# Kernel optimization log

Measured on AMD Instinct MI355X. Metric: run time of the kernel, lower is better.

The kernel has to match this reference:

```python
import jax, jax.numpy as jnp
import numpy as np

N = 30000
DEG = 16
E_RAND = N * DEG
E = E_RAND + N  # with self loops appended
T = 2
F_IN, H1, OUT = 128, 128, 64
NBSZ = 15
AGG = 0.8
NEG_SLOPE = 0.2


def setup_inputs() -> dict:
    key = jax.random.key(0)
    ks = jax.random.split(key, 10)
    x_all = jax.random.normal(ks[0], (T, N, F_IN), dtype=jnp.float32)
    # edges per snapshot: random edges + self loops (mirrors remove_self_loops + add_self_loops)
    loops = jnp.arange(N, dtype=jnp.int32)
    eis = []
    for t in range(T):
        src = jax.random.randint(jax.random.fold_in(ks[1], t), (E_RAND,), 0, N, dtype=jnp.int32)
        dst = jax.random.randint(jax.random.fold_in(ks[2], t), (E_RAND,), 0, N, dtype=jnp.int32)
        eis.append(jnp.stack([jnp.concatenate([src, loops]), jnp.concatenate([dst, loops])]))
    edge_index_all = jnp.stack(eis)  # [T, 2, E]
    def glorot(k, shape):
        fan = shape[0] + shape[-1]
        s = jnp.sqrt(6.0 / fan)
        return jax.random.uniform(k, shape, jnp.float32, -s, s)
    W1 = glorot(ks[3], (F_IN, 2 * H1))
    att1 = glorot(ks[4], (1, 1, 4 * H1))   # [1, heads=1, 2*out_neurons]
    b1 = jnp.zeros((2 * H1,), jnp.float32)
    W2 = glorot(ks[5], (H1, 2 * OUT))
    att2 = glorot(ks[6], (1, 1, 4 * OUT))
    b2 = jnp.zeros((2 * OUT,), jnp.float32)
    return {"x_all": x_all, "edge_index_all": edge_index_all,
            "W1": W1, "att1": att1, "b1": b1, "W2": W2, "att2": att2, "b2": b2}


def _conv(x, edge_index, W, att, b, C):
    """One DGIBConv (heads=1, Bernoulli distribution, diag reparam, eval mode).
    Returns (node_out [N,C], ixz scalar, structure_kl scalar)."""
    h = x @ W                                    # [N, 2C]
    src, dst = edge_index[0], edge_index[1]
    x_j = h[src]                                 # [E, 2C] per-edge gather (source)
    x_i = h[dst]                                 # [E, 2C] target
    a = att[0, 0]                                # [4C]
    logits = jnp.sum(x_i * a[:2 * C], -1) + jnp.sum(x_j * a[2 * C:], -1)  # [E]
    logits = jax.nn.leaky_relu(logits, NEG_SLOPE)
    # Bernoulli branch: softmax of ones over segments == 1/deg(dst)
    deg = jax.ops.segment_sum(jnp.ones_like(logits), dst, num_segments=N)  # [N]
    norm = 1.0 / deg[dst]
    p = jnp.clip(jax.nn.sigmoid(logits), 0.01, 0.99)  # posterior Bernoulli probs
    alpha = p * norm
    aggr = jax.ops.segment_sum(x_j * alpha[:, None], dst, num_segments=N) + b  # [N, 2C]
    # diag reparam: mean || std-logit split; Gaussian prior N(0, I)
    mu = aggr[:, :C]
    std = jax.nn.softplus(aggr[:, C:]) + 1e-10
    kl = -jnp.log(std) + 0.5 * (std * std + mu * mu) - 0.5  # KL(N(mu,std)||N(0,1)) per dim
    ixz = jnp.mean(jnp.sum(kl, -1))
    # structure KL: Bernoulli(p) || Bernoulli(logits = 1/nbsz)
    q = jax.nn.sigmoid(jnp.float32(1.0 / NBSZ))
    skl = jnp.mean(p * jnp.log(p / q) + (1.0 - p) * jnp.log((1.0 - p) / (1.0 - q)))
    return mu, ixz, skl


def _layer(x_list, edge_index_all, W, att, b, C):
    """Temporal DGIBConv.forward: per-snapshot conv + weighted temporal fusion."""
    outs, ixzs, skls = [], [], []
    for t in range(T):
        out, ixz, skl = _conv(x_list[t], edge_index_all[t], W, att, b, C)
        if t > 0:
            w = jax.nn.sigmoid(jnp.arange(t, dtype=jnp.float32))[:, None, None]  # [t,1,1]
            prev = jnp.stack(outs[:t])                                           # [t,N,C]
            out = jnp.sum(w * prev, 0) / t * AGG + out * (1.0 - AGG)
        outs.append(out)
        ixzs.append(ixz)
        skls.append(skl)
    return outs, jnp.mean(jnp.stack(ixzs)), jnp.mean(jnp.stack(skls))


def reference(x_all, edge_index_all, W1, att1, b1, W2, att2, b2):
    xs = [x_all[t] for t in range(T)]
    h1, ixz1, skl1 = _layer(xs, edge_index_all, W1, att1, b1, H1)
    h1 = [jax.nn.relu(h) for h in h1]  # with_relu=True, eval -> dropout is identity
    h2, ixz2, skl2 = _layer(h1, edge_index_all, W2, att2, b2, OUT)
    out = jnp.stack(h2)                # [T, N, OUT]
    ixz_mean = (ixz1 + ixz2) / 2.0
    skl_mean = (skl1 + skl2) / 2.0
    return out, ixz_mean, skl_mean
```

## Files before the change

### kernel.cpp

```cpp
#include <hip/hip_runtime.h>
#include <hip/hip_bf16.h>
#include <hip/hip_fp8.h>

#define N_NODES 30000
#define N_EDGES 510000
#define K_DIM   128
#define ABLK    7500

typedef short bf16x8 __attribute__((ext_vector_type(8)));
typedef float f32x4  __attribute__((ext_vector_type(4)));
typedef float f32x2  __attribute__((ext_vector_type(2)));
typedef unsigned int u32x2 __attribute__((ext_vector_type(2)));

__device__ __forceinline__ unsigned short f2bf(float f) {
  __hip_bfloat16 h = __float2bfloat16(f);
  return *(unsigned short*)&h;
}
__device__ __forceinline__ unsigned char f2fp8(float f) {
  __hip_fp8_e4m3 q(f);
  return (unsigned char)q.__x;
}

__global__ void transpose_w_kernel(const float* __restrict__ W1, unsigned short* __restrict__ Wt1,
                                   const float* __restrict__ W2, unsigned short* __restrict__ Wt2) {
  int i = blockIdx.x * blockDim.x + threadIdx.x;
  if (i < 128 * 256) {
    int k = i >> 8, m = i & 255;
    Wt1[m * 128 + k] = f2bf(W1[i]);
  } else if (i < 128 * 256 + 128 * 128) {
    int j = i - 128 * 256;
    int k = j >> 7, m = j & 127;
    Wt2[m * 128 + k] = f2bf(W2[j]);
  }
}

__global__ void deg_kernel(const int* __restrict__ ei, int* __restrict__ deg0,
                           int* __restrict__ deg1, int e) {
  int i = blockIdx.x * blockDim.x + threadIdx.x;
  if (i < 2 * e) {
    int t = i >= e ? 1 : 0;
    int j = i - t * e;
    int d = ei[(size_t)t * 2 * e + e + j];
    atomicAdd(&(t ? deg1 : deg0)[d], 1);
  }
}

__global__ __launch_bounds__(1024) void scan_kernel(const int* __restrict__ deg0, int* __restrict__ off0, int* __restrict__ cur0,
                                                    const int* __restrict__ deg1, int* __restrict__ off1, int* __restrict__ cur1,
                                                    int n) {
  const int* deg = blockIdx.x ? deg1 : deg0;
  int* off = blockIdx.x ? off1 : off0;
  int* cur = blockIdx.x ? cur1 : cur0;
  const int CHUNK = 30;
  __shared__ int wsum[16];
  int tid = threadIdx.x;
  int base = tid * CHUNK;
  int sum = 0;
  for (int i = 0; i < CHUNK; i++)
    if (base + i < n) sum += deg[base + i];
  int lane = tid & 63, wid = tid >> 6;
  int incl = sum;
#pragma unroll
  for (int o = 1; o < 64; o <<= 1) {
    int v = __shfl_up(incl, o);
    if (lane >= o) incl += v;
  }
  if (lane == 63) wsum[wid] = incl;
  __syncthreads();
  if (tid == 0) {
    int run = 0;
    for (int w = 0; w < 16; w++) { int v = wsum[w]; wsum[w] = run; run += v; }
  }
  __syncthreads();
  int run = incl - sum + wsum[wid];
  for (int i = 0; i < CHUNK; i++) {
    if (base + i < n) {
      off[base + i] = run;
      cur[base + i] = run;
      run += deg[base + i];
    }
  }
}

__global__ void scatter_kernel(const int* __restrict__ ei,
                               int* __restrict__ cur0, int* __restrict__ cur1,
                               int* __restrict__ csr0, int* __restrict__ csr1, int e) {
  int i = blockIdx.x * blockDim.x + threadIdx.x;
  if (i < 2 * e) {
    int t = i >= e ? 1 : 0;
    int j = i - t * e;
    int s = ei[(size_t)t * 2 * e + j];
    int d = ei[(size_t)t * 2 * e + e + j];
    int* cur = t ? cur1 : cur0;
    int* csr = t ? csr1 : csr0;
    int p = atomicAdd(&cur[d], 1);
    csr[p] = s;
  }
}

template<int M, bool F32IN>
__global__ __launch_bounds__(256) void gemm_kernel(const void* __restrict__ X0v,
                                                   const void* __restrict__ X1v,
                                                   const short* __restrict__ Wt,
                                                   unsigned char* __restrict__ H0,
                                                   unsigned char* __restrict__ H1,
                                                   const float* __restrict__ att,
                                                   float* __restrict__ si0, float* __restrict__ si1,
                                                   float* __restrict__ sj0, float* __restrict__ sj1,
                                                   int nrows) {
  int t = blockIdx.y;
  const void* Xv = t ? X1v : X0v;
  unsigned char* Hf8 = t ? H1 : H0;
  float* s_i = t ? si1 : si0;
  float* s_j = t ? sj1 : sj0;

  int wave = blockIdx.x * 4 + (threadIdx.x >> 6);
  int lane = threadIdx.x & 63;
  if (wave * 16 >= nrows) return;
  int m16 = lane & 15, quad = lane >> 4;

  bf16x8 a[4];
  size_t arow = (size_t)(wave * 16 + m16) * K_DIM + quad * 8;
  if constexpr (F32IN) {
    const float* X = (const float*)Xv;
#pragma unroll
    for (int kc = 0; kc < 4; kc++) {
      f32x4 lo = *(const f32x4*)(X + arow + kc * 32);
      f32x4 hi = *(const f32x4*)(X + arow + kc * 32 + 4);
#pragma unroll
      for (int j = 0; j < 4; j++) {
        ((unsigned short*)&a[kc])[j]     = f2bf(lo[j]);
        ((unsigned short*)&a[kc])[4 + j] = f2bf(hi[j]);
      }
    }
  } else {
    const short* X = (const short*)Xv;
#pragma unroll
    for (int kc = 0; kc < 4; kc++) a[kc] = *(const bf16x8*)(X + arow + kc * 32);
  }

  float sip[4] = {0.f, 0.f, 0.f, 0.f}, sjp[4] = {0.f, 0.f, 0.f, 0.f};
#pragma unroll
  for (int nt = 0; nt < M / 16; nt++) {
    f32x4 acc = {0.f, 0.f, 0.f, 0.f};
    size_t brow = (size_t)(nt * 16 + m16) * K_DIM + quad * 8;
#pragma unroll
    for (int kc = 0; kc < 4; kc++) {
      bf16x8 b = *(const bf16x8*)(Wt + brow + kc * 32);
      acc = __builtin_amdgcn_mfma_f32_16x16x32_bf16(a[kc], b, acc, 0, 0, 0);
    }
    int col = nt * 16 + m16;
    float aA = att[col], aB = att[M + col];
#pragma unroll
    for (int r = 0; r < 4; r++) {
      int row = wave * 16 + quad * 4 + r;
      Hf8[(size_t)row * M + col] = f2fp8(acc[r]);
      sip[r] += acc[r] * aA;
      sjp[r] += acc[r] * aB;
    }
  }
#pragma unroll
  for (int o = 1; o < 16; o <<= 1) {
#pragma unroll
    for (int r = 0; r < 4; r++) {
      sip[r] += __shfl_xor(sip[r], o);
      sjp[r] += __shfl_xor(sjp[r], o);
    }
  }
  if (m16 == 0) {
#pragma unroll
    for (int r = 0; r < 4; r++) {
      int row = wave * 16 + quad * 4 + r;
      s_i[row] = sip[r];
      s_j[row] = sjp[r];
    }
  }
}

template<int M>
__global__ __launch_bounds__(256) void aggr_kernel(const unsigned char* __restrict__ H0,
                                                   const unsigned char* __restrict__ H1,
                                                   const int* __restrict__ csr0, const int* __restrict__ csr1,
                                                   const int* __restrict__ off0, const int* __restrict__ off1,
                                                   const int* __restrict__ deg0, const int* __restrict__ deg1,
                                                   const float* __restrict__ si0, const float* __restrict__ si1,
                                                   const float* __restrict__ sj0, const float* __restrict__ sj1,
                                                   const float* __restrict__ bias,
                                                   float* __restrict__ mu0, float* __restrict__ mu1,
                                                   f32x2* __restrict__ partials,
                                                   int n) {
  constexpr int C = M / 2;
  constexpr int LPR = M / 8;
  constexpr int LOG2LPR = (M == 256) ? 5 : 4;
  constexpr int EPL = 64 / LPR;
  constexpr int NL = 4;
  constexpr int U = NL * EPL;

  int t = blockIdx.y;
  const unsigned char* Hf8 = t ? H1 : H0;
  const int* csr = t ? csr1 : csr0;
  const int* off = t ? off1 : off0;
  const int* deg = t ? deg1 : deg0;
  const float* s_i = t ? si1 : si0;
  const float* s_j = t ? sj1 : sj0;
  float* mu = t ? mu1 : mu0;

  __shared__ float red_i[4], red_s[4];
  int wid = threadIdx.x >> 6, lane = threadIdx.x & 63;
  int wave = blockIdx.x * 4 + wid;
  float ixz = 0.f, skl = 0.f;

  if (wave < n) {
    int d     = __builtin_amdgcn_readfirstlane(deg[wave]);
    int start = __builtin_amdgcn_readfirstlane(off[wave]);
    float si  = s_i[wave];
    float norm = 1.0f / (float)d;
    int sub = lane & (LPR - 1);
    int g   = lane >> LOG2LPR;
    int c0  = sub * 8;
    const float q   = 1.0f / (1.0f + __expf(-(1.0f / 15.0f)));
    const float lq  = __logf(q);
    const float l1q = __logf(1.0f - q);

    float acc[8];
#pragma unroll
    for (int k = 0; k < 8; k++) acc[k] = 0.f;

    for (int e0 = 0; e0 < d; e0 += U) {
      int ee = e0 + lane;
      bool val = (lane < U) && (ee < d);
      int ap = start + (val ? ee : (d - 1));
      int idxl = csr[ap];
      float sjl = s_j[idxl];
      float lg = si + sjl;
      lg = lg > 0.f ? lg : 0.2f * lg;
      float p = 1.0f / (1.0f + __expf(-lg));
      p = fminf(fmaxf(p, 0.01f), 0.99f);
      float wl = val ? p : 0.f;
      if (val)
        skl += p * (__logf(p) - lq) + (1.0f - p) * (__logf(1.0f - p) - l1q);

      u32x2 hv[NL];
      float wsel[NL];
#pragma unroll
      for (int l = 0; l < NL; l++) {
        int idx; float wv_;
        if constexpr (EPL == 2) {
          int i0 = __shfl(idxl, l * 2), i1 = __shfl(idxl, l * 2 + 1);
          float w0 = __shfl(wl, l * 2), w1 = __shfl(wl, l * 2 + 1);
          idx = g ? i1 : i0;
          wv_ = g ? w1 : w0;
        } else {
          int i0 = __shfl(idxl, l * 4),     i1 = __shfl(idxl, l * 4 + 1);
          int i2 = __shfl(idxl, l * 4 + 2), i3 = __shfl(idxl, l * 4 + 3);
          float w0 = __shfl(wl, l * 4),     w1 = __shfl(wl, l * 4 + 1);
          float w2 = __shfl(wl, l * 4 + 2), w3 = __shfl(wl, l * 4 + 3);
          int ia = (g & 1) ? i1 : i0, ib = (g & 1) ? i3 : i2;
          idx = (g & 2) ? ib : ia;
          float fa = (g & 1) ? w1 : w0, fb = (g & 1) ? w3 : w2;
          wv_ = (g & 2) ? fb : fa;
        }
        wsel[l] = wv_;
        hv[l] = *(const u32x2*)(Hf8 + (size_t)idx * M + c0);
      }
#pragma unroll
      for (int l = 0; l < NL; l++) {
        f32x2 d0 = __builtin_amdgcn_cvt_pk_f32_fp8((int)hv[l][0], false);
        f32x2 d1 = __builtin_amdgcn_cvt_pk_f32_fp8((int)hv[l][0], true);
        f32x2 d2 = __builtin_amdgcn_cvt_pk_f32_fp8((int)hv[l][1], false);
        f32x2 d3 = __builtin_amdgcn_cvt_pk_f32_fp8((int)hv[l][1], true);
        float wv_ = wsel[l];
        acc[0] += wv_ * d0[0]; acc[1] += wv_ * d0[1];
        acc[2] += wv_ * d1[0]; acc[3] += wv_ * d1[1];
        acc[4] += wv_ * d2[0]; acc[5] += wv_ * d2[1];
        acc[6] += wv_ * d3[0]; acc[7] += wv_ * d3[1];
      }
    }

#pragma unroll
    for (int o = LPR; o < 64; o <<= 1) {
#pragma unroll
      for (int k = 0; k < 8; k++) acc[k] += __shfl_xor(acc[k], o);
    }

    if (lane < LPR) {
      if (c0 < C) {
        f32x4 m0, m1;
#pragma unroll
        for (int k = 0; k < 4; k++) {
          float a = acc[k] * norm + bias[c0 + k];
          m0[k] = a;
          ixz += 0.5f * a * a - 0.5f;
        }
#pragma unroll
        for (int k = 0; k < 4; k++) {
          float a = acc[4 + k] * norm + bias[c0 + 4 + k];
          m1[k] = a;
          ixz += 0.5f * a * a - 0.5f;
        }
        *(f32x4*)(mu + (size_t)wave * C + c0) = m0;
        *(f32x4*)(mu + (size_t)wave * C + c0 + 4) = m1;
      } else {
#pragma unroll
        for (int k = 0; k < 8; k++) {
          float a = acc[k] * norm + bias[c0 + k];
          float sp = (a > 20.f) ? a : log1pf(__expf(a));
          sp += 1e-10f;
          ixz += -__logf(sp) + 0.5f * sp * sp;
        }
      }
    }
  }
#pragma unroll
  for (int o = 32; o > 0; o >>= 1) {
    ixz += __shfl_xor(ixz, o);
    skl += __shfl_xor(skl, o);
  }
  if (lane == 0) { red_i[wid] = ixz; red_s[wid] = skl; }
  __syncthreads();
  if (threadIdx.x == 0) {
    f32x2 pr;
    pr[0] = red_i[0] + red_i[1] + red_i[2] + red_i[3];
    pr[1] = red_s[0] + red_s[1] + red_s[2] + red_s[3];
    partials[t * ABLK + blockIdx.x] = pr;
  }
}

__global__ void fuse1_kernel(const float* __restrict__ mu0, const float* __restrict__ mu1,
                             __hip_bfloat16* __restrict__ x0, __hip_bfloat16* __restrict__ x1, int n) {
  int i = blockIdx.x * blockDim.x + threadIdx.x;
  if (i < n) {
    float m0 = mu0[i], m1 = mu1[i];
    x0[i] = __float2bfloat16(fmaxf(m0, 0.f));
    x1[i] = __float2bfloat16(fmaxf(0.4f * m0 + 0.2f * m1, 0.f));
  }
}

__global__ void fuse2_kernel(const float* __restrict__ mu0, const float* __restrict__ mu1,
                             float* __restrict__ out, int n) {
  int i = blockIdx.x * blockDim.x + threadIdx.x;
  if (i < n) {
    float m0 = mu0[i], m1 = mu1[i];
    out[i] = m0;
    out[n + i] = 0.4f * m0 + 0.2f * m1;
  }
}

__global__ __launch_bounds__(1024) void reduce_kernel(const f32x2* __restrict__ p1,
                                                      const f32x2* __restrict__ p2,
                                                      float* __restrict__ out2) {
  __shared__ float ri[16], rs[16];
  float ixz = 0.f, skl = 0.f;
  for (int i = threadIdx.x; i < 2 * ABLK; i += 1024) {
    f32x2 a = p1[i], b = p2[i];
    ixz += a[0] + b[0];
    skl += a[1] + b[1];
  }
  int lane = threadIdx.x & 63, wid = threadIdx.x >> 6;
#pragma unroll
  for (int o = 32; o > 0; o >>= 1) {
    ixz += __shfl_xor(ixz, o);
    skl += __shfl_xor(skl, o);
  }
  if (lane == 0) { ri[wid] = ixz; rs[wid] = skl; }
  __syncthreads();
  if (threadIdx.x == 0) {
    float si = 0.f, ss = 0.f;
    for (int w = 0; w < 16; w++) { si += ri[w]; ss += rs[w]; }
    out2[0] = si / (4.0f * (float)N_NODES);
    out2[1] = ss / (4.0f * (float)N_EDGES);
  }
}

extern "C" void kernel_launch(void* const* d_in, const int* in_sizes, int n_in,
                              void* d_out, int out_size, void* d_ws, size_t ws_size,
                              hipStream_t stream) {
  const float* x_all = (const float*)d_in[0];
  const int* ei      = (const int*)d_in[1];
  const float* W1    = (const float*)d_in[2];
  const float* att1  = (const float*)d_in[3];
  const float* b1    = (const float*)d_in[4];
  const float* W2    = (const float*)d_in[5];
  const float* att2  = (const float*)d_in[6];
  const float* b2    = (const float*)d_in[7];
  float* out         = (float*)d_out;

  char* ws = (char*)d_ws;
  size_t off = 0;
  auto alloc = [&](size_t bytes) {
    char* p = ws + off;
    off = (off + bytes + 255) & ~(size_t)255;
    return p;
  };
  unsigned short* wt1  = (unsigned short*)alloc(256 * 128 * sizeof(short));
  unsigned short* wt2  = (unsigned short*)alloc(128 * 128 * sizeof(short));
  unsigned char* hf8_0 = (unsigned char*)alloc((size_t)N_NODES * 256);
  unsigned char* hf8_1 = (unsigned char*)alloc((size_t)N_NODES * 256);
  float* si0   = (float*)alloc(N_NODES * sizeof(float));
  float* si1   = (float*)alloc(N_NODES * sizeof(float));
  float* sj0   = (float*)alloc(N_NODES * sizeof(float));
  float* sj1   = (float*)alloc(N_NODES * sizeof(float));
  float* mu1_0 = (float*)alloc((size_t)N_NODES * 128 * sizeof(float));
  float* mu1_1 = (float*)alloc((size_t)N_NODES * 128 * sizeof(float));
  __hip_bfloat16* x2_0 = (__hip_bfloat16*)alloc((size_t)N_NODES * 128 * sizeof(short));
  __hip_bfloat16* x2_1 = (__hip_bfloat16*)alloc((size_t)N_NODES * 128 * sizeof(short));
  float* mu2_0 = mu1_0;
  float* mu2_1 = mu1_0 + (size_t)N_NODES * 64;
  int* degp[2]  = {(int*)alloc(N_NODES * 4), (int*)alloc(N_NODES * 4)};
  int* offp[2]  = {(int*)alloc(N_NODES * 4), (int*)alloc(N_NODES * 4)};
  int* curp[2]  = {(int*)alloc(N_NODES * 4), (int*)alloc(N_NODES * 4)};
  int* csrp[2]  = {(int*)alloc(N_EDGES * 4), (int*)alloc(N_EDGES * 4)};
  f32x2* part1  = (f32x2*)alloc(2 * ABLK * sizeof(f32x2));
  f32x2* part2  = (f32x2*)alloc(2 * ABLK * sizeof(f32x2));

  hipMemsetAsync(degp[0], 0, N_NODES * 4, stream);
  hipMemsetAsync(degp[1], 0, N_NODES * 4, stream);

  transpose_w_kernel<<<192, 256, 0, stream>>>(W1, wt1, W2, wt2);

  deg_kernel<<<(2 * N_EDGES + 255) / 256, 256, 0, stream>>>(ei, degp[0], degp[1], N_EDGES);
  scan_kernel<<<2, 1024, 0, stream>>>(degp[0], offp[0], curp[0], degp[1], offp[1], curp[1], N_NODES);
  scatter_kernel<<<(2 * N_EDGES + 255) / 256, 256, 0, stream>>>(ei, curp[0], curp[1],
                                                                csrp[0], csrp[1], N_EDGES);

  dim3 ggrid(469, 2), agrid(ABLK, 2);

  const float* x0 = x_all;
  const float* x1 = x_all + (size_t)N_NODES * K_DIM;
  gemm_kernel<256, true><<<ggrid, 256, 0, stream>>>(x0, x1, (const short*)wt1, hf8_0, hf8_1,
                                                    att1, si0, si1, sj0, sj1, N_NODES);
  aggr_kernel<256><<<agrid, 256, 0, stream>>>(hf8_0, hf8_1, csrp[0], csrp[1], offp[0], offp[1],
                                              degp[0], degp[1], si0, si1, sj0, sj1, b1,
                                              mu1_0, mu1_1, part1, N_NODES);
  fuse1_kernel<<<(N_NODES * 128 + 255) / 256, 256, 0, stream>>>(mu1_0, mu1_1, x2_0, x2_1, N_NODES * 128);

  gemm_kernel<128, false><<<ggrid, 256, 0, stream>>>(x2_0, x2_1, (const short*)wt2, hf8_0, hf8_1,
                                                     att2, si0, si1, sj0, sj1, N_NODES);
  aggr_kernel<128><<<agrid, 256, 0, stream>>>(hf8_0, hf8_1, csrp[0], csrp[1], offp[0], offp[1],
                                              degp[0], degp[1], si0, si1, sj0, sj1, b2,
                                              mu2_0, mu2_1, part2, N_NODES);
  fuse2_kernel<<<(N_NODES * 64 + 255) / 256, 256, 0, stream>>>(mu2_0, mu2_1, out, N_NODES * 64);
  reduce_kernel<<<1, 1024, 0, stream>>>(part1, part2, out + (size_t)2 * N_NODES * 64);
}
```

Baseline: 602.6 us.

## Split edge weight computation into separate edge kernel and pipeline aggregation loads

After: 811.6 us. 34.7% more time.

```diff
diff --git a/kernel.cpp b/kernel.cpp
--- a/kernel.cpp
+++ b/kernel.cpp
@@ -1,11 +1,11 @@
 #include <hip/hip_runtime.h>
 #include <hip/hip_bf16.h>
-#include <hip/hip_fp8.h>
 
 #define N_NODES 30000
 #define N_EDGES 510000
 #define K_DIM   128
 #define ABLK    7500
+#define EBLK    997
 
 typedef short bf16x8 __attribute__((ext_vector_type(8)));
 typedef float f32x4  __attribute__((ext_vector_type(4)));
@@ -15,10 +15,6 @@
 __device__ __forceinline__ unsigned short f2bf(float f) {
   __hip_bfloat16 h = __float2bfloat16(f);
   return *(unsigned short*)&h;
-}
-__device__ __forceinline__ unsigned char f2fp8(float f) {
-  __hip_fp8_e4m3 q(f);
-  return (unsigned char)q.__x;
 }
 
 __global__ void transpose_w_kernel(const float* __restrict__ W1, unsigned short* __restrict__ Wt1,
@@ -45,12 +41,15 @@
   }
 }
 
-__global__ __launch_bounds__(1024) void scan_kernel(const int* __restrict__ deg0, int* __restrict__ off0, int* __restrict__ cur0,
-                                                    const int* __restrict__ deg1, int* __restrict__ off1, int* __restrict__ cur1,
+__global__ __launch_bounds__(1024) void scan_kernel(const int* __restrict__ deg0, int* __restrict__ off0,
+                                                    int* __restrict__ cur0, float* __restrict__ rn0,
+                                                    const int* __restrict__ deg1, int* __restrict__ off1,
+                                                    int* __restrict__ cur1, float* __restrict__ rn1,
                                                     int n) {
   const int* deg = blockIdx.x ? deg1 : deg0;
   int* off = blockIdx.x ? off1 : off0;
   int* cur = blockIdx.x ? cur1 : cur0;
+  float* rn = blockIdx.x ? rn1 : rn0;
   const int CHUNK = 30;
   __shared__ int wsum[16];
   int tid = threadIdx.x;
@@ -75,16 +74,18 @@
   int run = incl - sum + wsum[wid];
   for (int i = 0; i < CHUNK; i++) {
     if (base + i < n) {
+      int dg = deg[base + i];
       off[base + i] = run;
       cur[base + i] = run;
-      run += deg[base + i];
+      rn[base + i] = 1.0f / (float)dg;
+      run += dg;
     }
   }
 }
 
 __global__ void scatter_kernel(const int* __restrict__ ei,
                                int* __restrict__ cur0, int* __restrict__ cur1,
-                               int* __restrict__ csr0, int* __restrict__ csr1, int e) {
+                               unsigned int* __restrict__ csr0, unsigned int* __restrict__ csr1, int e) {
   int i = blockIdx.x * blockDim.x + threadIdx.x;
   if (i < 2 * e) {
     int t = i >= e ? 1 : 0;
@@ -92,9 +93,9 @@
     int s = ei[(size_t)t * 2 * e + j];
     int d = ei[(size_t)t * 2 * e + e + j];
     int* cur = t ? cur1 : cur0;
-    int* csr = t ? csr1 : csr0;
+    unsigned int* csr = t ? csr1 : csr0;
     int p = atomicAdd(&cur[d], 1);
-    csr[p] = s;
+    csr[p] = (unsigned int)s | ((unsigned int)d << 16);
   }
 }
 
@@ -154,7 +155,8 @@
 #pragma unroll
     for (int r = 0; r < 4; r++) {
       int row = wave * 16 + quad * 4 + r;
-      Hf8[(size_t)row * M + col] = f2fp8(acc[r]);
+      int pk = __builtin_amdgcn_cvt_pk_fp8_f32(acc[r], acc[r], 0, false);
+      Hf8[(size_t)row * M + col] = (unsigned char)pk;
       sip[r] += acc[r] * aA;
       sjp[r] += acc[r] * aB;
     }
@@ -177,153 +179,196 @@
   }
 }
 
+__global__ __launch_bounds__(256) void edge_kernel(const unsigned int* __restrict__ csr_0,
+                                                   const unsigned int* __restrict__ csr_1,
+                                                   const float* __restrict__ rn0, const float* __restrict__ rn1,
+                                                   const float* __restrict__ si0, const float* __restrict__ si1,
+                                                   const float* __restrict__ sj0, const float* __restrict__ sj1,
+                                                   u32x2* __restrict__ iw0, u32x2* __restrict__ iw1,
+                                                   float* __restrict__ epart,
+                                                   int e) {
+  int t = blockIdx.y;
+  const unsigned int* csr = t ? csr_1 : csr_0;
+  const float* rn = t ? rn1 : rn0;
+  const float* s_i = t ? si1 : si0;
+  const float* s_j = t ? sj1 : sj0;
+  u32x2* iw = t ? iw1 : iw0;
+
+  const float q   = 1.0f / (1.0f + __expf(-(1.0f / 15.0f)));
+  const float lq  = __logf(q);
+  const float l1q = __logf(1.0f - q);
+
+  __shared__ float red[4];
+  float skl = 0.f;
+  int p0 = (blockIdx.x * 256 + threadIdx.x) * 2;
+#pragma unroll
+  for (int u = 0; u < 2; u++) {
+    int p = p0 + u;
+    if (p < e) {
+      unsigned int sd = csr[p];
+      int s = (int)(sd & 0xffffu);
+      int dd = (int)(sd >> 16);
+      float lg = s_i[dd] + s_j[s];
+      lg = lg > 0.f ? lg : 0.2f * lg;
+      float pv = 1.0f / (1.0f + __expf(-lg));
+      pv = fminf(fmaxf(pv, 0.01f), 0.99f);
+      skl += pv * (__logf(pv) - lq) + (1.0f - pv) * (__logf(1.0f - pv) - l1q);
+      float w = pv * rn[dd];
+      u32x2 o;
+      o[0] = (unsigned int)s;
+      o[1] = __float_as_uint(w);
+      iw[p] = o;
+    }
+  }
+  int lane = threadIdx.x & 63, wid = threadIdx.x >> 6;
+#pragma unroll
+  for (int o = 32; o > 0; o >>= 1) skl += __shfl_xor(skl, o);
+  if (lane == 0) red[wid] = skl;
+  __syncthreads();
+  if (threadIdx.x == 0) epart[t * EBLK + blockIdx.x] = red[0] + red[1] + red[2] + red[3];
+}
+
 template<int M>
 __global__ __launch_bounds__(256) void aggr_kernel(const unsigned char* __restrict__ H0,
                                                    const unsigned char* __restrict__ H1,
-                                                   const int* __restrict__ csr0, const int* __restrict__ csr1,
+                                                   const u32x2* __restrict__ iw0, const u32x2* __restrict__ iw1,
                                                    const int* __restrict__ off0, const int* __restrict__ off1,
                                                    const int* __restrict__ deg0, const int* __restrict__ deg1,
-                                                   const float* __restrict__ si0, const float* __restrict__ si1,
-                                                   const float* __restrict__ sj0, const float* __restrict__ sj1,
                                                    const float* __restrict__ bias,
                                                    float* __restrict__ mu0, float* __restrict__ mu1,
-                                                   f32x2* __restrict__ partials,
+                                                   float* __restrict__ apart,
                                                    int n) {
   constexpr int C = M / 2;
-  constexpr int LPR = M / 8;
-  constexpr int LOG2LPR = (M == 256) ? 5 : 4;
+  constexpr int LPR = M / 16;
+  constexpr int L2LPR = (M == 256) ? 4 : 3;
   constexpr int EPL = 64 / LPR;
-  constexpr int NL = 4;
-  constexpr int U = NL * EPL;
-
-  int t = blockIdx.y;
+  constexpr int U = 16;
+  constexpr int NL = U / EPL;
+
+  int bid = blockIdx.x;
+  int xcd = bid & 7;
+  int t = xcd >> 2;
+  int nb = (bid >> 3) * 4 + (xcd & 3);
+
   const unsigned char* Hf8 = t ? H1 : H0;
-  const int* csr = t ? csr1 : csr0;
+  const u32x2* iw = t ? iw1 : iw0;
   const int* off = t ? off1 : off0;
   const int* deg = t ? deg1 : deg0;
-  const float* s_i = t ? si1 : si0;
-  const float* s_j = t ? sj1 : sj0;
   float* mu = t ? mu1 : mu0;
 
-  __shared__ float red_i[4], red_s[4];
+  __shared__ float red_i[4];
   int wid = threadIdx.x >> 6, lane = threadIdx.x & 63;
-  int wave = blockIdx.x * 4 + wid;
-  float ixz = 0.f, skl = 0.f;
+  int wave = nb * 4 + wid;
+  float ixz = 0.f;
 
   if (wave < n) {
     int d     = __builtin_amdgcn_readfirstlane(deg[wave]);
     int start = __builtin_amdgcn_readfirstlane(off[wave]);
-    float si  = s_i[wave];
-    float norm = 1.0f / (float)d;
+    const u32x2* iwp = iw + start;
     int sub = lane & (LPR - 1);
-    int g   = lane >> LOG2LPR;
-    int c0  = sub * 8;
-    const float q   = 1.0f / (1.0f + __expf(-(1.0f / 15.0f)));
-    const float lq  = __logf(q);
-    const float l1q = __logf(1.0f - q);
-
-    float acc[8];
-#pragma unroll
-    for (int k = 0; k < 8; k++) acc[k] = 0.f;
-
-    for (int e0 = 0; e0 < d; e0 += U) {
-      int ee = e0 + lane;
-      bool val = (lane < U) && (ee < d);
-      int ap = start + (val ? ee : (d - 1));
-      int idxl = csr[ap];
-      float sjl = s_j[idxl];
-      float lg = si + sjl;
-      lg = lg > 0.f ? lg : 0.2f * lg;
-      float p = 1.0f / (1.0f + __expf(-lg));
-      p = fminf(fmaxf(p, 0.01f), 0.99f);
-      float wl = val ? p : 0.f;
-      if (val)
-        skl += p * (__logf(p) - lq) + (1.0f - p) * (__logf(1.0f - p) - l1q);
-
-      u32x2 hv[NL];
-      float wsel[NL];
+    int g   = lane >> L2LPR;
+    int c0  = sub * 16;
+    const unsigned char* hbase = Hf8 + c0;
+
+    f32x2 acc[8];
+#pragma unroll
+    for (int k = 0; k < 8; k++) acc[k] = {0.f, 0.f};
+
+    u32x2 iwr[NL];
+    uint4 hv0[NL], hv1[NL];
+    float w0[NL], w1[NL];
+
+    auto LOADIW = [&](int base) {
 #pragma unroll
       for (int l = 0; l < NL; l++) {
-        int idx; float wv_;
-        if constexpr (EPL == 2) {
-          int i0 = __shfl(idxl, l * 2), i1 = __shfl(idxl, l * 2 + 1);
-          float w0 = __shfl(wl, l * 2), w1 = __shfl(wl, l * 2 + 1);
-          idx = g ? i1 : i0;
-          wv_ = g ? w1 : w0;
-        } else {
-          int i0 = __shfl(idxl, l * 4),     i1 = __shfl(idxl, l * 4 + 1);
-          int i2 = __shfl(idxl, l * 4 + 2), i3 = __shfl(idxl, l * 4 + 3);
-          float w0 = __shfl(wl, l * 4),     w1 = __shfl(wl, l * 4 + 1);
-          float w2 = __shfl(wl, l * 4 + 2), w3 = __shfl(wl, l * 4 + 3);
-          int ia = (g & 1) ? i1 : i0, ib = (g & 1) ? i3 : i2;
-          idx = (g & 2) ? ib : ia;
-          float fa = (g & 1) ? w1 : w0, fb = (g & 1) ? w3 : w2;
-          wv_ = (g & 2) ? fb : fa;
+        int e = base + l * EPL + g;
+        e = e < d ? e : d - 1;
+        iwr[l] = iwp[e];
+      }
+    };
+    auto ISSUE = [&](uint4* hv) {
+#pragma unroll
+      for (int l = 0; l < NL; l++)
+        hv[l] = *(const uint4*)(hbase + (size_t)iwr[l][0] * M);
+    };
+    auto EXTW = [&](float* w, int base) {
+#pragma unroll
+      for (int l = 0; l < NL; l++) {
+        int e = base + l * EPL + g;
+        w[l] = (e < d) ? __uint_as_float(iwr[l][1]) : 0.f;
+      }
+    };
+    auto FMA = [&](uint4* hv, float* w) {
+#pragma unroll
+      for (int l = 0; l < NL; l++) {
+        f32x2 wv = {w[l], w[l]};
+#pragma unroll
+        for (int k = 0; k < 4; k++) {
+          f32x2 lo = __builtin_amdgcn_cvt_pk_f32_fp8((int)hv[l][k], false);
+          f32x2 hi = __builtin_amdgcn_cvt_pk_f32_fp8((int)hv[l][k], true);
+          acc[2 * k]     = lo * wv + acc[2 * k];
+          acc[2 * k + 1] = hi * wv + acc[2 * k + 1];
         }
-        wsel[l] = wv_;
-        hv[l] = *(const u32x2*)(Hf8 + (size_t)idx * M + c0);
-      }
-#pragma unroll
-      for (int l = 0; l < NL; l++) {
-        f32x2 d0 = __builtin_amdgcn_cvt_pk_f32_fp8((int)hv[l][0], false);
-        f32x2 d1 = __builtin_amdgcn_cvt_pk_f32_fp8((int)hv[l][0], true);
-        f32x2 d2 = __builtin_amdgcn_cvt_pk_f32_fp8((int)hv[l][1], false);
-        f32x2 d3 = __builtin_amdgcn_cvt_pk_f32_fp8((int)hv[l][1], true);
-        float wv_ = wsel[l];
-        acc[0] += wv_ * d0[0]; acc[1] += wv_ * d0[1];
-        acc[2] += wv_ * d1[0]; acc[3] += wv_ * d1[1];
-        acc[4] += wv_ * d2[0]; acc[5] += wv_ * d2[1];
-        acc[6] += wv_ * d3[0]; acc[7] += wv_ * d3[1];
-      }
+      }
+    };
+
+    int nch = (d + U - 1) / U;
+    LOADIW(0);
+    ISSUE(hv0); EXTW(w0, 0);
+    LOADIW(U);
+    int c = 0;
+    while (true) {
+      if (c + 1 < nch) { ISSUE(hv1); EXTW(w1, (c + 1) * U); LOADIW((c + 2) * U); }
+      FMA(hv0, w0);
+      if (++c >= nch) break;
+      if (c + 1 < nch) { ISSUE(hv0); EXTW(w0, (c + 1) * U); LOADIW((c + 2) * U); }
+      FMA(hv1, w1);
+      if (++c >= nch) break;
     }
 
 #pragma unroll
     for (int o = LPR; o < 64; o <<= 1) {
 #pragma unroll
-      for (int k = 0; k < 8; k++) acc[k] += __shfl_xor(acc[k], o);
+      for (int j = 0; j < 8; j++) {
+        acc[j][0] += __shfl_xor(acc[j][0], o);
+        acc[j][1] += __shfl_xor(acc[j][1], o);
+      }
     }
 
     if (lane < LPR) {
       if (c0 < C) {
-        f32x4 m0, m1;
-#pragma unroll
-        for (int k = 0; k < 4; k++) {
-          float a = acc[k] * norm + bias[c0 + k];
-          m0[k] = a;
-          ixz += 0.5f * a * a - 0.5f;
+        f32x4 mv[4];
+#pragma unroll
+        for (int j = 0; j < 8; j++) {
+          float a0 = acc[j][0] + bias[c0 + 2 * j];
+          float a1 = acc[j][1] + bias[c0 + 2 * j + 1];
+          ixz += 0.5f * (a0 * a0 + a1 * a1) - 1.0f;
+          mv[j >> 1][(j & 1) * 2]     = a0;
+          mv[j >> 1][(j & 1) * 2 + 1] = a1;
         }
 #pragma unroll
-        for (int k = 0; k < 4; k++) {
-          float a = acc[4 + k] * norm + bias[c0 + 4 + k];
-          m1[k] = a;
-          ixz += 0.5f * a * a - 0.5f;
+        for (int k = 0; k < 4; k++)
+          *(f32x4*)(mu + (size_t)wave * C + c0 + 4 * k) = mv[k];
+      } else {
+#pragma unroll
+        for (int j = 0; j < 8; j++) {
+#pragma unroll
+          for (int h = 0; h < 2; h++) {
+            float a = acc[j][h] + bias[c0 + 2 * j + h];
+            float sp = (a > 20.f) ? a : log1pf(__expf(a));
+            sp += 1e-10f;
+            ixz += -__logf(sp) + 0.5f * sp * sp;
+          }
         }
-        *(f32x4*)(mu + (size_t)wave * C + c0) = m0;
-        *(f32x4*)(mu + (size_t)wave * C + c0 + 4) = m1;
-      } else {
-#pragma unroll
-        for (int k = 0; k < 8; k++) {
-          float a = acc[k] * norm + bias[c0 + k];
-          float sp = (a > 20.f) ? a : log1pf(__expf(a));
-          sp += 1e-10f;
-          ixz += -__logf(sp) + 0.5f * sp * sp;
-        }
-      }
-    }
-  }
-#pragma unroll
-  for (int o = 32; o > 0; o >>= 1) {
-    ixz += __shfl_xor(ixz, o);
-    skl += __shfl_xor(skl, o);
-  }
-  if (lane == 0) { red_i[wid] = ixz; red_s[wid] = skl; }
+      }
+    }
+  }
+#pragma unroll
+  for (int o = 32; o > 0; o >>= 1) ixz += __shfl_xor(ixz, o);
+  if (lane == 0) red_i[wid] = ixz;
   __syncthreads();
-  if (threadIdx.x == 0) {
-    f32x2 pr;
-    pr[0] = red_i[0] + red_i[1] + red_i[2] + red_i[3];
-    pr[1] = red_s[0] + red_s[1] + red_s[2] + red_s[3];
-    partials[t * ABLK + blockIdx.x] = pr;
-  }
+  if (threadIdx.x == 0)
+    apart[t * ABLK + nb] = red_i[0] + red_i[1] + red_i[2] + red_i[3];
 }
 
 __global__ void fuse1_kernel(const float* __restrict__ mu0, const float* __restrict__ mu1,
@@ -346,16 +391,15 @@
   }
 }
 
-__global__ __launch_bounds__(1024) void reduce_kernel(const f32x2* __restrict__ p1,
-                                                      const f32x2* __restrict__ p2,
+__global__ __launch_bounds__(1024) void reduce_kernel(const float* __restrict__ a1,
+                                                      const float* __restrict__ a2,
+                                                      const float* __restrict__ e1,
+                                                      const float* __restrict__ e2,
                                                       float* __restrict__ out2) {
   __shared__ float ri[16], rs[16];
   float ixz = 0.f, skl = 0.f;
-  for (int i = threadIdx.x; i < 2 * ABLK; i += 1024) {
-    f32x2 a = p1[i], b = p2[i];
-    ixz += a[0] + b[0];
-    skl += a[1] + b[1];
-  }
+  for (int i = threadIdx.x; i < 2 * ABLK; i += 1024) ixz += a1[i] + a2[i];
+  for (int i = threadIdx.x; i < 2 * EBLK; i += 1024) skl += e1[i] + e2[i];
   int lane = threadIdx.x & 63, wid = threadIdx.x >> 6;
 #pragma unroll
   for (int o = 32; o > 0; o >>= 1) {
@@ -402,16 +446,22 @@
   float* sj1   = (float*)alloc(N_NODES * sizeof(float));
   float* mu1_0 = (float*)alloc((size_t)N_NODES * 128 * sizeof(float));
   float* mu1_1 = (float*)alloc((size_t)N_NODES * 128 * sizeof(float));
-  __hip_bfloat16* x2_0 = (__hip_bfloat16*)alloc((size_t)N_NODES * 128 * sizeof(short));
-  __hip_bfloat16* x2_1 = (__hip_bfloat16*)alloc((size_t)N_NODES * 128 * sizeof(short));
+  char* x2region = alloc((size_t)N_NODES * 256 * sizeof(short));
+  __hip_bfloat16* x2_0 = (__hip_bfloat16*)x2region;
+  __hip_bfloat16* x2_1 = x2_0 + (size_t)N_NODES * 128;
+  u32x2* iwp[2] = {(u32x2*)x2region, (u32x2*)x2region + N_EDGES};
   float* mu2_0 = mu1_0;
   float* mu2_1 = mu1_0 + (size_t)N_NODES * 64;
   int* degp[2]  = {(int*)alloc(N_NODES * 4), (int*)alloc(N_NODES * 4)};
   int* offp[2]  = {(int*)alloc(N_NODES * 4), (int*)alloc(N_NODES * 4)};
   int* curp[2]  = {(int*)alloc(N_NODES * 4), (int*)alloc(N_NODES * 4)};
-  int* csrp[2]  = {(int*)alloc(N_EDGES * 4), (int*)alloc(N_EDGES * 4)};
-  f32x2* part1  = (f32x2*)alloc(2 * ABLK * sizeof(f32x2));
-  f32x2* part2  = (f32x2*)alloc(2 * ABLK * sizeof(f32x2));
+  float* rnp[2] = {(float*)alloc(N_NODES * 4), (float*)alloc(N_NODES * 4)};
+  unsigned int* csrp[2] = {(unsigned int*)alloc((size_t)N_EDGES * 4),
+                           (unsigned int*)alloc((size_t)N_EDGES * 4)};
+  float* apart1 = (float*)alloc(2 * ABLK * sizeof(float));
+  float* apart2 = (float*)alloc(2 * ABLK * sizeof(float));
+  float* epart1 = (float*)alloc(2 * EBLK * sizeof(float));
+  float* epart2 = (float*)alloc(2 * EBLK * sizeof(float));
 
   hipMemsetAsync(degp[0], 0, N_NODES * 4, stream);
   hipMemsetAsync(degp[1], 0, N_NODES * 4, stream);
@@ -419,26 +469,29 @@
   transpose_w_kernel<<<192, 256, 0, stream>>>(W1, wt1, W2, wt2);
 
   deg_kernel<<<(2 * N_EDGES + 255) / 256, 256, 0, stream>>>(ei, degp[0], degp[1], N_EDGES);
-  scan_kernel<<<2, 1024, 0, stream>>>(degp[0], offp[0], curp[0], degp[1], offp[1], curp[1], N_NODES);
+  scan_kernel<<<2, 1024, 0, stream>>>(degp[0], offp[0], curp[0], rnp[0],
+                                      degp[1], offp[1], curp[1], rnp[1], N_NODES);
   scatter_kernel<<<(2 * N_EDGES + 255) / 256, 256, 0, stream>>>(ei, curp[0], curp[1],
                                                                 csrp[0], csrp[1], N_EDGES);
 
-  dim3 ggrid(469, 2), agrid(ABLK, 2);
+  dim3 ggrid(469, 2), egrid(EBLK, 2);
 
   const float* x0 = x_all;
   const float* x1 = x_all + (size_t)N_NODES * K_DIM;
   gemm_kernel<256, true><<<ggrid, 256, 0, stream>>>(x0, x1, (const short*)wt1, hf8_0, hf8_1,
                                                     att1, si0, si1, sj0, sj1, N_NODES);
-  aggr_kernel<256><<<agrid, 256, 0, stream>>>(hf8_0, hf8_1, csrp[0], csrp[1], offp[0], offp[1],
-                                              degp[0], degp[1], si0, si1, sj0, sj1, b1,
-                                              mu1_0, mu1_1, part1, N_NODES);
+  edge_kernel<<<egrid, 256, 0, stream>>>(csrp[0], csrp[1], rnp[0], rnp[1],
+                                         si0, si1, sj0, sj1, iwp[0], iwp[1], epart1, N_EDGES);
+  aggr_kernel<256><<<2 * ABLK, 256, 0, stream>>>(hf8_0, hf8_1, iwp[0], iwp[1], offp[0], offp[1],
+                                                 degp[0], degp[1], b1, mu1_0, mu1_1, apart1, N_NODES);
   fuse1_kernel<<<(N_NODES * 128 + 255) / 256, 256, 0, stream>>>(mu1_0, mu1_1, x2_0, x2_1, N_NODES * 128);
 
   gemm_kernel<128, false><<<ggrid, 256, 0, stream>>>(x2_0, x2_1, (const short*)wt2, hf8_0, hf8_1,
                                                      att2, si0, si1, sj0, sj1, N_NODES);
-  aggr_kernel<128><<<agrid, 256, 0, stream>>>(hf8_0, hf8_1, csrp[0], csrp[1], offp[0], offp[1],
-                                              degp[0], degp[1], si0, si1, sj0, sj1, b2,
-                                              mu2_0, mu2_1, part2, N_NODES);
+  edge_kernel<<<egrid, 256, 0, stream>>>(csrp[0], csrp[1], rnp[0], rnp[1],
+                                         si0, si1, sj0, sj1, iwp[0], iwp[1], epart2, N_EDGES);
+  aggr_kernel<128><<<2 * ABLK, 256, 0, stream>>>(hf8_0, hf8_1, iwp[0], iwp[1], offp[0], offp[1],
+                                                 degp[0], degp[1], b2, mu2_0, mu2_1, apart2, N_NODES);
   fuse2_kernel<<<(N_NODES * 64 + 255) / 256, 256, 0, stream>>>(mu2_0, mu2_1, out, N_NODES * 64);
-  reduce_kernel<<<1, 1024, 0, stream>>>(part1, part2, out + (size_t)2 * N_NODES * 64);
-}
+  reduce_kernel<<<1, 1024, 0, stream>>>(apart1, apart2, epart1, epart2, out + (size_t)2 * N_NODES * 64);
+}
```
